# Performance work log

Hardware: AMD Instinct MI355X
Metric: run time of the kernel (lower is better)

## Reference

```python
import jax, jax.numpy as jnp
import numpy as np

D_MODEL = 1024
NUM_HEADS = 16
HEAD_DIM = D_MODEL // NUM_HEADS


def setup_inputs() -> dict:
    key = jax.random.key(0)
    k1, k2, k3, k4, k5 = jax.random.split(key, 5)
    B, S = 2, 2048
    X = jax.random.normal(k1, (B, S, D_MODEL), dtype=jnp.float32)
    Wqkv = jax.random.normal(k2, (3 * D_MODEL, D_MODEL), dtype=jnp.float32) * 0.02
    bqkv = jax.random.normal(k3, (3 * D_MODEL,), dtype=jnp.float32) * 0.02
    Wo = jax.random.normal(k4, (D_MODEL, D_MODEL), dtype=jnp.float32) * 0.02
    bo = jax.random.normal(k5, (D_MODEL,), dtype=jnp.float32) * 0.02
    return {"X": X, "Wqkv": Wqkv, "bqkv": bqkv, "Wo": Wo, "bo": bo}


def reference(X, Wqkv, bqkv, Wo, bo):
    B, S, D = X.shape
    # fused QKV projection (torch Linear: x @ W.T + b)
    qkv = X @ Wqkv.T + bqkv                                  # [B, S, 3D]
    qkv = qkv.reshape(B, S, NUM_HEADS, 3 * HEAD_DIM)
    qkv = jnp.transpose(qkv, (0, 2, 1, 3))                   # [B, H, S, 3*hd]
    q, k, v = jnp.split(qkv, 3, axis=-1)                     # each [B, H, S, hd]
    # naive scaled dot-product attention (materializes full SxS scores)
    scale = 1.0 / jnp.sqrt(jnp.asarray(HEAD_DIM, dtype=X.dtype))
    scores = jnp.einsum("bhqd,bhkd->bhqk", q, k) * scale     # [B, H, S, S]
    attn = jax.nn.softmax(scores, axis=-1)
    values = jnp.einsum("bhqk,bhkd->bhqd", attn, v)          # [B, H, S, hd]
    values = jnp.transpose(values, (0, 2, 1, 3)).reshape(B, S, D)
    return values @ Wo.T + bo
```

## Files before the change

### kernel.cpp

```cpp
#include <hip/hip_runtime.h>

#define DM    1024
#define NH    16
#define HD    64
#define SEQ   2048
#define BATCH 2
#define NQKV  3072
#define MTOT  4096

using half2v = __attribute__((ext_vector_type(2))) _Float16;
using half4  = __attribute__((ext_vector_type(4))) _Float16;
using half8  = __attribute__((ext_vector_type(8))) _Float16;
using f32x4  = __attribute__((ext_vector_type(4))) float;

typedef const __attribute__((address_space(1))) unsigned int* gp_t;
typedef __attribute__((address_space(3))) unsigned int* lp_t;

__device__ __forceinline__ void gl2lds16(const void* g, void* l) {
    __builtin_amdgcn_global_load_lds((gp_t)g, (lp_t)l, 16, 0, 0);
}

__device__ __forceinline__ f32x4 fzero4() {
    f32x4 v; v[0] = 0.f; v[1] = 0.f; v[2] = 0.f; v[3] = 0.f; return v;
}

__device__ __forceinline__ int sw8(int row, int col) {
    return (row << 6) | ((((col >> 3) ^ row) & 7) << 3) | (col & 7);
}

#define CSCALE 0.18033688011112042f

__device__ __forceinline__ half2v expp2(float a, float b) {
    return __builtin_bit_cast(half2v, __builtin_amdgcn_cvt_pkrtz(
        __builtin_amdgcn_exp2f(a), __builtin_amdgcn_exp2f(b)));
}

__global__ __launch_bounds__(256) void cvt_all(const float* __restrict__ X,
                                               const float* __restrict__ W1,
                                               const float* __restrict__ W2,
                                               const float* __restrict__ bqkv,
                                               float* __restrict__ bscaled,
                                               _Float16* __restrict__ out) {
    const int nX = MTOT * DM / 4, nW1 = NQKV * DM / 4, nW2 = DM * DM / 4;
    int i = blockIdx.x * 256 + threadIdx.x;
    if (i < NQKV) {
        const float b = bqkv[i];
        bscaled[i] = ((i % 192) < 64) ? b * CSCALE : b;
    }
    if (i >= nX + nW1 + nW2) return;
    float4 f;
    float sc = 1.0f;
    if (i < nX) {
        f = reinterpret_cast<const float4*>(X)[i];
    } else if (i < nX + nW1) {
        const int off = i - nX;
        f = reinterpret_cast<const float4*>(W1)[off];
        const int row = off >> 8;
        if ((row % 192) < 64) sc = CSCALE;
    } else {
        f = reinterpret_cast<const float4*>(W2)[i - nX - nW1];
    }
    half4 h;
    h[0] = (_Float16)(f.x * sc); h[1] = (_Float16)(f.y * sc);
    h[2] = (_Float16)(f.z * sc); h[3] = (_Float16)(f.w * sc);
    reinterpret_cast<half4*>(out)[i] = h;
}

template <bool OUT_F16, bool FUSE_V>
__global__ __launch_bounds__(256) void gemm_nt(const _Float16* __restrict__ A,
                                               const _Float16* __restrict__ B,
                                               const float* __restrict__ bias,
                                               void* __restrict__ Cout,
                                               _Float16* __restrict__ vtout,
                                               int M, int N, int K) {
    __shared__ _Float16 lA[128 * 64];
    __shared__ _Float16 lB[128 * 64];
    const int tid = threadIdx.x;
    const int m0 = blockIdx.y * 128, n0 = blockIdx.x * 128;
    const int wave = tid >> 6, lane = tid & 63, quad = lane >> 4, l15 = lane & 15;
    const int wm = (wave & 1) * 64, wn = (wave >> 1) * 64;

    f32x4 acc[4][4];
#pragma unroll
    for (int i = 0; i < 4; ++i)
#pragma unroll
        for (int j = 0; j < 4; ++j) acc[i][j] = fzero4();

    const int cperm = (((tid & 7) ^ (tid >> 3)) & 7) * 8;
    const _Float16* Ab = A + (long)(m0 + (tid >> 3)) * K + cperm;
    const _Float16* Bb = B + (long)(n0 + (tid >> 3)) * K + cperm;
    char* lAp = (char*)lA + tid * 16;
    char* lBp = (char*)lB + tid * 16;

    for (int kt = 0; kt < K; kt += 64) {
        __syncthreads();
#pragma unroll
        for (int j = 0; j < 4; ++j) {
            gl2lds16(Ab + (long)j * 32 * K + kt, lAp + j * 4096);
            gl2lds16(Bb + (long)j * 32 * K + kt, lBp + j * 4096);
        }
        __syncthreads();
#pragma unroll
        for (int ks = 0; ks < 2; ++ks) {
            half8 af[4], bfr[4];
#pragma unroll
            for (int t = 0; t < 4; ++t) {
                af[t]  = *(const half8*)(lA + sw8(wm + t * 16 + l15, ks * 32 + quad * 8));
                bfr[t] = *(const half8*)(lB + sw8(wn + t * 16 + l15, ks * 32 + quad * 8));
            }
#pragma unroll
            for (int mt = 0; mt < 4; ++mt)
#pragma unroll
                for (int nt = 0; nt < 4; ++nt)
                    acc[mt][nt] = __builtin_amdgcn_mfma_f32_16x16x32_f16(
                        af[mt], bfr[nt], acc[mt][nt], 0, 0, 0);
        }
    }

    float bs[4];
#pragma unroll
    for (int nt = 0; nt < 4; ++nt) bs[nt] = bias[n0 + wn + nt * 16 + l15];

#pragma unroll
    for (int nt = 0; nt < 4; ++nt) {
        const int nbase = n0 + wn + nt * 16;
        if (FUSE_V && (nbase % 192) >= 128) {
            const int h = nbase / 192;
            const int d = (nbase % 192) - 128 + l15;
            _Float16* vrow = vtout + ((long)((nbase / 192) * 0 + h) * HD + d) * SEQ;
#pragma unroll
            for (int mt = 0; mt < 4; ++mt) {
                const int mbase = m0 + wm + mt * 16;
                const int bb = mbase >> 11;
                const int sbase = mbase & (SEQ - 1);
                const int pos = (sbase & ~31) + 8 * quad + 4 * ((sbase >> 4) & 1);
                half4 hv;
#pragma unroll
                for (int r = 0; r < 4; ++r) hv[r] = (_Float16)(acc[mt][nt][r] + bs[nt]);
                *(half4*)(vrow + (long)bb * NH * HD * SEQ + pos) = hv;
            }
        } else {
#pragma unroll
            for (int mt = 0; mt < 4; ++mt) {
#pragma unroll
                for (int r = 0; r < 4; ++r) {
                    const int m = m0 + wm + mt * 16 + quad * 4 + r;
                    const int n = nbase + l15;
                    const float v = acc[mt][nt][r] + bs[nt];
                    if constexpr (OUT_F16)
                        ((_Float16*)Cout)[(long)m * N + n] = (_Float16)v;
                    else
                        ((float*)Cout)[(long)m * N + n] = v;
                }
            }
        }
    }
}

template <bool OUT_F16>
__global__ __launch_bounds__(256) void gemm_nt_64(const _Float16* __restrict__ A,
                                                  const _Float16* __restrict__ B,
                                                  const float* __restrict__ bias,
                                                  void* __restrict__ Cout,
                                                  int M, int N, int K) {
    __shared__ _Float16 lA[64 * 64];
    __shared__ _Float16 lB[128 * 64];
    const int tid = threadIdx.x;
    const int m0 = blockIdx.y * 64, n0 = blockIdx.x * 128;
    const int wave = tid >> 6, lane = tid & 63, quad = lane >> 4, l15 = lane & 15;
    const int wm = (wave & 1) * 32, wn = (wave >> 1) * 64;

    f32x4 acc[2][4];
#pragma unroll
    for (int i = 0; i < 2; ++i)
#pragma unroll
        for (int j = 0; j < 4; ++j) acc[i][j] = fzero4();

    const int cperm = (((tid & 7) ^ (tid >> 3)) & 7) * 8;
    const _Float16* Ab = A + (long)(m0 + (tid >> 3)) * K + cperm;
    const _Float16* Bb = B + (long)(n0 + (tid >> 3)) * K + cperm;
    char* lAp = (char*)lA + tid * 16;
    char* lBp = (char*)lB + tid * 16;

    for (int kt = 0; kt < K; kt += 64) {
        __syncthreads();
#pragma unroll
        for (int j = 0; j < 2; ++j)
            gl2lds16(Ab + (long)j * 32 * K + kt, lAp + j * 4096);
#pragma unroll
        for (int j = 0; j < 4; ++j)
            gl2lds16(Bb + (long)j * 32 * K + kt, lBp + j * 4096);
        __syncthreads();
#pragma unroll
        for (int ks = 0; ks < 2; ++ks) {
            half8 af[2], bfr[4];
#pragma unroll
            for (int t = 0; t < 2; ++t)
                af[t] = *(const half8*)(lA + sw8(wm + t * 16 + l15, ks * 32 + quad * 8));
#pragma unroll
            for (int t = 0; t < 4; ++t)
                bfr[t] = *(const half8*)(lB + sw8(wn + t * 16 + l15, ks * 32 + quad * 8));
#pragma unroll
            for (int mt = 0; mt < 2; ++mt)
#pragma unroll
                for (int nt = 0; nt < 4; ++nt)
                    acc[mt][nt] = __builtin_amdgcn_mfma_f32_16x16x32_f16(
                        af[mt], bfr[nt], acc[mt][nt], 0, 0, 0);
        }
    }

    float bs[4];
#pragma unroll
    for (int nt = 0; nt < 4; ++nt) bs[nt] = bias[n0 + wn + nt * 16 + l15];

#pragma unroll
    for (int mt = 0; mt < 2; ++mt) {
#pragma unroll
        for (int r = 0; r < 4; ++r) {
            const int m = m0 + wm + mt * 16 + quad * 4 + r;
#pragma unroll
            for (int nt = 0; nt < 4; ++nt) {
                const int n = n0 + wn + nt * 16 + l15;
                const float v = acc[mt][nt][r] + bs[nt];
                if constexpr (OUT_F16)
                    ((_Float16*)Cout)[(long)m * N + n] = (_Float16)v;
                else
                    ((float*)Cout)[(long)m * N + n] = v;
            }
        }
    }
}

__global__ __launch_bounds__(256) void attn_flash(const _Float16* __restrict__ qkv,
                                                  const _Float16* __restrict__ vt,
                                                  _Float16* __restrict__ aout) {
    __shared__ _Float16 lKV[4][64 * 64];

    const int L = blockIdx.x;
    const int c = L & 7, j = L >> 3;
    const int pair = c * 4 + (j >> 5);
    const int b = pair >> 4, h = pair & 15;
    const int q0 = (j & 31) * 64;

    const int tid = threadIdx.x;
    const int wave = tid >> 6, lane = tid & 63, quad = lane >> 4, l15 = lane & 15;
    const int cperm8 = (((tid & 7) ^ (tid >> 3)) & 7) * 8;

    const _Float16* qsrc = qkv + (long)(b * SEQ + q0 + (tid >> 3)) * NQKV + h * 192 + cperm8;
#pragma unroll
    for (int jq = 0; jq < 2; ++jq)
        gl2lds16(qsrc + (long)jq * 32 * NQKV, (char*)lKV + jq * 4096 + tid * 16);
    __syncthreads();

    half8 qf[2];
#pragma unroll
    for (int ks = 0; ks < 2; ++ks)
        qf[ks] = *(const half8*)(lKV[0] + sw8(wave * 16 + l15, ks * 32 + quad * 8));
    __syncthreads();

    f32x4 O[4];
#pragma unroll
    for (int dt = 0; dt < 4; ++dt) O[dt] = fzero4();
    f32x4 lsum = fzero4();

    half8 ones;
#pragma unroll
    for (int i = 0; i < 8; ++i) ones[i] = (_Float16)1.0f;

    const _Float16* ksrc = qkv + (long)(b * SEQ + (tid >> 3)) * NQKV + h * 192 + 64 + cperm8;
    const _Float16* vsrc = vt + (long)((b * NH + h) * HD + (tid >> 3)) * SEQ + cperm8;

#pragma unroll
    for (int jj = 0; jj < 2; ++jj) {
        gl2lds16(ksrc + (long)(jj * 32) * NQKV, (char*)lKV[0] + jj * 4096 + tid * 16);
        gl2lds16(vsrc + (long)(jj * 32) * SEQ,  (char*)lKV[2] + jj * 4096 + tid * 16);
    }
    __syncthreads();

    for (int it = 0; it < 32; ++it) {
        const int cur = it & 1;
        if (it < 31) {
            const int s0n = (it + 1) * 64;
#pragma unroll
            for (int jj = 0; jj < 2; ++jj) {
                gl2lds16(ksrc + (long)(s0n + jj * 32) * NQKV, (char*)lKV[cur ^ 1] + jj * 4096 + tid * 16);
                gl2lds16(vsrc + (long)(jj * 32) * SEQ + s0n,  (char*)lKV[2 + (cur ^ 1)] + jj * 4096 + tid * 16);
            }
        }
        const _Float16* lK = lKV[cur];
        const _Float16* lV = lKV[2 + cur];

#pragma unroll
        for (int t = 0; t < 2; ++t) {
            f32x4 s[2];
            s[0] = fzero4(); s[1] = fzero4();
#pragma unroll
            for (int tt = 0; tt < 2; ++tt) {
#pragma unroll
                for (int ks = 0; ks < 2; ++ks) {
                    half8 kf = *(const half8*)(lK + sw8((2 * t + tt) * 16 + l15, ks * 32 + quad * 8));
                    s[tt] = __builtin_amdgcn_mfma_f32_16x16x32_f16(kf, qf[ks], s[tt], 0, 0, 0);
                }
            }
            half2v p01 = expp2(s[0][0], s[0][1]);
            half2v p23 = expp2(s[0][2], s[0][3]);
            half2v p45 = expp2(s[1][0], s[1][1]);
            half2v p67 = expp2(s[1][2], s[1][3]);
            half4 lo = __builtin_shufflevector(p01, p23, 0, 1, 2, 3);
            half4 hi = __builtin_shufflevector(p45, p67, 0, 1, 2, 3);
            half8 pf = __builtin_shufflevector(lo, hi, 0, 1, 2, 3, 4, 5, 6, 7);
            lsum = __builtin_amdgcn_mfma_f32_16x16x32_f16(pf, ones, lsum, 0, 0, 0);
#pragma unroll
            for (int dt = 0; dt < 4; ++dt) {
                half8 vf = *(const half8*)(lV + sw8(dt * 16 + l15, t * 32 + quad * 8));
                O[dt] = __builtin_amdgcn_mfma_f32_16x16x32_f16(pf, vf, O[dt], 0, 0, 0);
            }
        }
        __syncthreads();
    }

#pragma unroll
    for (int r = 0; r < 4; ++r) {
        const float lr = 1.0f / lsum[r];
        const int row = b * SEQ + q0 + wave * 16 + quad * 4 + r;
#pragma unroll
        for (int dt = 0; dt < 4; ++dt)
            aout[(long)row * DM + h * HD + dt * 16 + l15] =
                (_Float16)(O[dt][r] * lr);
    }
}

extern "C" void kernel_launch(void* const* d_in, const int* in_sizes, int n_in,
                              void* d_out, int out_size, void* d_ws, size_t ws_size,
                              hipStream_t stream) {
    const float* X    = (const float*)d_in[0];
    const float* Wqkv = (const float*)d_in[1];
    const float* bqkv = (const float*)d_in[2];
    const float* Wo   = (const float*)d_in[3];
    const float* bo   = (const float*)d_in[4];

    char* ws = (char*)d_ws;
    _Float16* Xh   = (_Float16*)(ws);
    _Float16* Wqh  = (_Float16*)(ws + (size_t)8  * 1048576);
    _Float16* Woh  = (_Float16*)(ws + (size_t)14 * 1048576);
    _Float16* qkvh = (_Float16*)(ws + (size_t)16 * 1048576);
    _Float16* vth  = (_Float16*)(ws + (size_t)40 * 1048576);
    _Float16* atth = (_Float16*)(ws + (size_t)48 * 1048576);
    float* bscaled = (float*)(ws + (size_t)48 * 1048576);

    const int ncvt = (MTOT * DM + NQKV * DM + DM * DM) / 4;
    cvt_all<<<(ncvt + 255) / 256, 256, 0, stream>>>(X, Wqkv, Wo, bqkv, bscaled, Xh);

    gemm_nt<true, true><<<dim3(NQKV / 128, MTOT / 128), 256, 0, stream>>>(
        Xh, Wqh, bscaled, qkvh, vth, MTOT, NQKV, DM);

    attn_flash<<<1024, 256, 0, stream>>>(qkvh, vth, atth);

    gemm_nt_64<false><<<dim3(DM / 128, MTOT / 64), 256, 0, stream>>>(
        atth, Woh, bo, d_out, MTOT, DM, DM);
}
```

Baseline: 187.2 us.

## Switch attention kernel to 32x32x16 MFMA with split-K across wave pairs

Rewrites the flash attention inner loop to use 32x32x16 MFMA tiles. Each pair of waves shares a 32-row query tile and splits each 64-key block in half, and the two partial O and row-sum accumulators are reduced through LDS at the end. The V-transpose layout written by the QKV GEMM epilogue is changed to match the new B-operand fragment order. The aim is to cut LDS fragment reads and instruction count per FLOP, at the cost of a final cross-wave reduction, more accumulator registers, and only half the waves doing the output stores.

```diff
diff --git a/kernel.cpp b/kernel.cpp
--- a/kernel.cpp
+++ b/kernel.cpp
@@ -12,6 +12,7 @@
 using half4  = __attribute__((ext_vector_type(4))) _Float16;
 using half8  = __attribute__((ext_vector_type(8))) _Float16;
 using f32x4  = __attribute__((ext_vector_type(4))) float;
+using f32x16 = __attribute__((ext_vector_type(16))) float;
 
 typedef const __attribute__((address_space(1))) unsigned int* gp_t;
 typedef __attribute__((address_space(3))) unsigned int* lp_t;
@@ -22,6 +23,12 @@
 
 __device__ __forceinline__ f32x4 fzero4() {
     f32x4 v; v[0] = 0.f; v[1] = 0.f; v[2] = 0.f; v[3] = 0.f; return v;
+}
+__device__ __forceinline__ f32x16 fzero16() {
+    f32x16 v;
+#pragma unroll
+    for (int i = 0; i < 16; ++i) v[i] = 0.f;
+    return v;
 }
 
 __device__ __forceinline__ int sw8(int row, int col) {
@@ -127,13 +134,13 @@
         if (FUSE_V && (nbase % 192) >= 128) {
             const int h = nbase / 192;
             const int d = (nbase % 192) - 128 + l15;
-            _Float16* vrow = vtout + ((long)((nbase / 192) * 0 + h) * HD + d) * SEQ;
+            _Float16* vrow = vtout + ((long)h * HD + d) * SEQ;
 #pragma unroll
             for (int mt = 0; mt < 4; ++mt) {
                 const int mbase = m0 + wm + mt * 16;
                 const int bb = mbase >> 11;
                 const int sbase = mbase & (SEQ - 1);
-                const int pos = (sbase & ~31) + 8 * quad + 4 * ((sbase >> 4) & 1);
+                const int pos = sbase + 8 * (quad & 1) + 4 * (quad >> 1);
                 half4 hv;
 #pragma unroll
                 for (int r = 0; r < 4; ++r) hv[r] = (_Float16)(acc[mt][nt][r] + bs[nt]);
@@ -243,7 +250,9 @@
     const int q0 = (j & 31) * 64;
 
     const int tid = threadIdx.x;
-    const int wave = tid >> 6, lane = tid & 63, quad = lane >> 4, l15 = lane & 15;
+    const int wave = tid >> 6, lane = tid & 63;
+    const int l31 = lane & 31, hi = lane >> 5;
+    const int qt = wave >> 1, kh = wave & 1;
     const int cperm8 = (((tid & 7) ^ (tid >> 3)) & 7) * 8;
 
     const _Float16* qsrc = qkv + (long)(b * SEQ + q0 + (tid >> 3)) * NQKV + h * 192 + cperm8;
@@ -252,16 +261,14 @@
         gl2lds16(qsrc + (long)jq * 32 * NQKV, (char*)lKV + jq * 4096 + tid * 16);
     __syncthreads();
 
-    half8 qf[2];
-#pragma unroll
-    for (int ks = 0; ks < 2; ++ks)
-        qf[ks] = *(const half8*)(lKV[0] + sw8(wave * 16 + l15, ks * 32 + quad * 8));
+    half8 qf[4];
+#pragma unroll
+    for (int ks = 0; ks < 4; ++ks)
+        qf[ks] = *(const half8*)(lKV[0] + sw8(32 * qt + l31, ks * 16 + hi * 8));
     __syncthreads();
 
-    f32x4 O[4];
-#pragma unroll
-    for (int dt = 0; dt < 4; ++dt) O[dt] = fzero4();
-    f32x4 lsum = fzero4();
+    f32x16 O[2] = {fzero16(), fzero16()};
+    f32x16 lsum = fzero16();
 
     half8 ones;
 #pragma unroll
@@ -290,43 +297,76 @@
         const _Float16* lK = lKV[cur];
         const _Float16* lV = lKV[2 + cur];
 
-#pragma unroll
-        for (int t = 0; t < 2; ++t) {
-            f32x4 s[2];
-            s[0] = fzero4(); s[1] = fzero4();
-#pragma unroll
-            for (int tt = 0; tt < 2; ++tt) {
-#pragma unroll
-                for (int ks = 0; ks < 2; ++ks) {
-                    half8 kf = *(const half8*)(lK + sw8((2 * t + tt) * 16 + l15, ks * 32 + quad * 8));
-                    s[tt] = __builtin_amdgcn_mfma_f32_16x16x32_f16(kf, qf[ks], s[tt], 0, 0, 0);
-                }
-            }
-            half2v p01 = expp2(s[0][0], s[0][1]);
-            half2v p23 = expp2(s[0][2], s[0][3]);
-            half2v p45 = expp2(s[1][0], s[1][1]);
-            half2v p67 = expp2(s[1][2], s[1][3]);
+        f32x16 st = fzero16();
+#pragma unroll
+        for (int ks = 0; ks < 4; ++ks) {
+            half8 kf = *(const half8*)(lK + sw8(32 * kh + l31, ks * 16 + hi * 8));
+            st = __builtin_amdgcn_mfma_f32_32x32x16_f16(kf, qf[ks], st, 0, 0, 0);
+        }
+
+#pragma unroll
+        for (int kc = 0; kc < 2; ++kc) {
+            half2v p01 = expp2(st[8 * kc + 0], st[8 * kc + 1]);
+            half2v p23 = expp2(st[8 * kc + 2], st[8 * kc + 3]);
+            half2v p45 = expp2(st[8 * kc + 4], st[8 * kc + 5]);
+            half2v p67 = expp2(st[8 * kc + 6], st[8 * kc + 7]);
             half4 lo = __builtin_shufflevector(p01, p23, 0, 1, 2, 3);
-            half4 hi = __builtin_shufflevector(p45, p67, 0, 1, 2, 3);
-            half8 pf = __builtin_shufflevector(lo, hi, 0, 1, 2, 3, 4, 5, 6, 7);
-            lsum = __builtin_amdgcn_mfma_f32_16x16x32_f16(pf, ones, lsum, 0, 0, 0);
-#pragma unroll
-            for (int dt = 0; dt < 4; ++dt) {
-                half8 vf = *(const half8*)(lV + sw8(dt * 16 + l15, t * 32 + quad * 8));
-                O[dt] = __builtin_amdgcn_mfma_f32_16x16x32_f16(pf, vf, O[dt], 0, 0, 0);
+            half4 hp = __builtin_shufflevector(p45, p67, 0, 1, 2, 3);
+            half8 pf = __builtin_shufflevector(lo, hp, 0, 1, 2, 3, 4, 5, 6, 7);
+            lsum = __builtin_amdgcn_mfma_f32_32x32x16_f16(pf, ones, lsum, 0, 0, 0);
+#pragma unroll
+            for (int dt = 0; dt < 2; ++dt) {
+                half8 vf = *(const half8*)(lV + sw8(32 * dt + l31, kh * 32 + kc * 16 + hi * 8));
+                O[dt] = __builtin_amdgcn_mfma_f32_32x32x16_f16(pf, vf, O[dt], 0, 0, 0);
             }
         }
         __syncthreads();
     }
 
-#pragma unroll
-    for (int r = 0; r < 4; ++r) {
-        const float lr = 1.0f / lsum[r];
-        const int row = b * SEQ + q0 + wave * 16 + quad * 4 + r;
-#pragma unroll
-        for (int dt = 0; dt < 4; ++dt)
-            aout[(long)row * DM + h * HD + dt * 16 + l15] =
-                (_Float16)(O[dt][r] * lr);
+    float* red = (float*)lKV;
+    if (kh) {
+#pragma unroll
+        for (int dt = 0; dt < 2; ++dt)
+#pragma unroll
+            for (int cc = 0; cc < 4; ++cc) {
+                f32x4 v;
+#pragma unroll
+                for (int i = 0; i < 4; ++i) v[i] = O[dt][4 * cc + i];
+                *(f32x4*)(red + ((qt * 12 + dt * 4 + cc) * 256) + lane * 4) = v;
+            }
+#pragma unroll
+        for (int cc = 0; cc < 4; ++cc) {
+            f32x4 v;
+#pragma unroll
+            for (int i = 0; i < 4; ++i) v[i] = lsum[4 * cc + i];
+            *(f32x4*)(red + ((qt * 12 + 8 + cc) * 256) + lane * 4) = v;
+        }
+    }
+    __syncthreads();
+    if (!kh) {
+#pragma unroll
+        for (int dt = 0; dt < 2; ++dt)
+#pragma unroll
+            for (int cc = 0; cc < 4; ++cc) {
+                f32x4 v = *(const f32x4*)(red + ((qt * 12 + dt * 4 + cc) * 256) + lane * 4);
+#pragma unroll
+                for (int i = 0; i < 4; ++i) O[dt][4 * cc + i] += v[i];
+            }
+#pragma unroll
+        for (int cc = 0; cc < 4; ++cc) {
+            f32x4 v = *(const f32x4*)(red + ((qt * 12 + 8 + cc) * 256) + lane * 4);
+#pragma unroll
+            for (int i = 0; i < 4; ++i) lsum[4 * cc + i] += v[i];
+        }
+#pragma unroll
+        for (int r = 0; r < 16; ++r) {
+            const float lr = 1.0f / lsum[r];
+            const int row = b * SEQ + q0 + 32 * qt + (r & 3) + 8 * (r >> 2) + 4 * hi;
+#pragma unroll
+            for (int dt = 0; dt < 2; ++dt)
+                aout[(long)row * DM + h * HD + 32 * dt + l31] =
+                    (_Float16)(O[dt][r] * lr);
+        }
     }
 }
 
```

Result: slower. 193.7 us (+3.4%).

## Double-buffer LDS tiles in GEMMs and shrink QKV GEMM M-tile to 64

Applied to the files above, without the earlier changes.

Replaces both GEMM kernels with one double-buffered variant that prefetches the next K-slice into a second LDS buffer while MFMAs run on the current one, leaving one barrier per iteration. The QKV projection moves from 128x128 to 64x128 tiles, which doubles its block count and lowers per-block accumulator registers. In exchange, each block reuses its loaded B tile across fewer rows, so global and L2 traffic rises, and LDS per block grows to hold two buffers.

```diff
diff --git a/kernel.cpp b/kernel.cpp
--- a/kernel.cpp
+++ b/kernel.cpp
@@ -67,54 +67,66 @@
 }
 
 template <bool OUT_F16, bool FUSE_V>
-__global__ __launch_bounds__(256) void gemm_nt(const _Float16* __restrict__ A,
+__global__ __launch_bounds__(256) void gemm_db(const _Float16* __restrict__ A,
                                                const _Float16* __restrict__ B,
                                                const float* __restrict__ bias,
                                                void* __restrict__ Cout,
                                                _Float16* __restrict__ vtout,
                                                int M, int N, int K) {
-    __shared__ _Float16 lA[128 * 64];
-    __shared__ _Float16 lB[128 * 64];
+    __shared__ _Float16 lA[2][64 * 64];
+    __shared__ _Float16 lB[2][128 * 64];
     const int tid = threadIdx.x;
-    const int m0 = blockIdx.y * 128, n0 = blockIdx.x * 128;
+    const int m0 = blockIdx.y * 64, n0 = blockIdx.x * 128;
     const int wave = tid >> 6, lane = tid & 63, quad = lane >> 4, l15 = lane & 15;
-    const int wm = (wave & 1) * 64, wn = (wave >> 1) * 64;
-
-    f32x4 acc[4][4];
-#pragma unroll
-    for (int i = 0; i < 4; ++i)
+    const int wm = (wave & 1) * 32, wn = (wave >> 1) * 64;
+
+    f32x4 acc[2][4];
+#pragma unroll
+    for (int i = 0; i < 2; ++i)
 #pragma unroll
         for (int j = 0; j < 4; ++j) acc[i][j] = fzero4();
 
     const int cperm = (((tid & 7) ^ (tid >> 3)) & 7) * 8;
     const _Float16* Ab = A + (long)(m0 + (tid >> 3)) * K + cperm;
     const _Float16* Bb = B + (long)(n0 + (tid >> 3)) * K + cperm;
-    char* lAp = (char*)lA + tid * 16;
-    char* lBp = (char*)lB + tid * 16;
-
-    for (int kt = 0; kt < K; kt += 64) {
-        __syncthreads();
-#pragma unroll
-        for (int j = 0; j < 4; ++j) {
-            gl2lds16(Ab + (long)j * 32 * K + kt, lAp + j * 4096);
-            gl2lds16(Bb + (long)j * 32 * K + kt, lBp + j * 4096);
-        }
-        __syncthreads();
+
+#pragma unroll
+    for (int j = 0; j < 2; ++j)
+        gl2lds16(Ab + (long)j * 32 * K, (char*)lA[0] + j * 4096 + tid * 16);
+#pragma unroll
+    for (int j = 0; j < 4; ++j)
+        gl2lds16(Bb + (long)j * 32 * K, (char*)lB[0] + j * 4096 + tid * 16);
+    __syncthreads();
+
+    const int KI = K >> 6;
+    for (int it = 0; it < KI; ++it) {
+        const int cur = it & 1;
+        if (it + 1 < KI) {
+            const int kt = (it + 1) * 64;
+#pragma unroll
+            for (int j = 0; j < 2; ++j)
+                gl2lds16(Ab + (long)j * 32 * K + kt, (char*)lA[cur ^ 1] + j * 4096 + tid * 16);
+#pragma unroll
+            for (int j = 0; j < 4; ++j)
+                gl2lds16(Bb + (long)j * 32 * K + kt, (char*)lB[cur ^ 1] + j * 4096 + tid * 16);
+        }
 #pragma unroll
         for (int ks = 0; ks < 2; ++ks) {
-            half8 af[4], bfr[4];
-#pragma unroll
-            for (int t = 0; t < 4; ++t) {
-                af[t]  = *(const half8*)(lA + sw8(wm + t * 16 + l15, ks * 32 + quad * 8));
-                bfr[t] = *(const half8*)(lB + sw8(wn + t * 16 + l15, ks * 32 + quad * 8));
-            }
-#pragma unroll
-            for (int mt = 0; mt < 4; ++mt)
+            half8 af[2], bfr[4];
+#pragma unroll
+            for (int t = 0; t < 2; ++t)
+                af[t] = *(const half8*)(lA[cur] + sw8(wm + t * 16 + l15, ks * 32 + quad * 8));
+#pragma unroll
+            for (int t = 0; t < 4; ++t)
+                bfr[t] = *(const half8*)(lB[cur] + sw8(wn + t * 16 + l15, ks * 32 + quad * 8));
+#pragma unroll
+            for (int mt = 0; mt < 2; ++mt)
 #pragma unroll
                 for (int nt = 0; nt < 4; ++nt)
                     acc[mt][nt] = __builtin_amdgcn_mfma_f32_16x16x32_f16(
                         af[mt], bfr[nt], acc[mt][nt], 0, 0, 0);
         }
+        __syncthreads();
     }
 
     float bs[4];
@@ -127,9 +139,9 @@
         if (FUSE_V && (nbase % 192) >= 128) {
             const int h = nbase / 192;
             const int d = (nbase % 192) - 128 + l15;
-            _Float16* vrow = vtout + ((long)((nbase / 192) * 0 + h) * HD + d) * SEQ;
-#pragma unroll
-            for (int mt = 0; mt < 4; ++mt) {
+            _Float16* vrow = vtout + ((long)h * HD + d) * SEQ;
+#pragma unroll
+            for (int mt = 0; mt < 2; ++mt) {
                 const int mbase = m0 + wm + mt * 16;
                 const int bb = mbase >> 11;
                 const int sbase = mbase & (SEQ - 1);
@@ -141,7 +153,7 @@
             }
         } else {
 #pragma unroll
-            for (int mt = 0; mt < 4; ++mt) {
+            for (int mt = 0; mt < 2; ++mt) {
 #pragma unroll
                 for (int r = 0; r < 4; ++r) {
                     const int m = m0 + wm + mt * 16 + quad * 4 + r;
@@ -157,80 +169,6 @@
     }
 }
 
-template <bool OUT_F16>
-__global__ __launch_bounds__(256) void gemm_nt_64(const _Float16* __restrict__ A,
-                                                  const _Float16* __restrict__ B,
-                                                  const float* __restrict__ bias,
-                                                  void* __restrict__ Cout,
-                                                  int M, int N, int K) {
-    __shared__ _Float16 lA[64 * 64];
-    __shared__ _Float16 lB[128 * 64];
-    const int tid = threadIdx.x;
-    const int m0 = blockIdx.y * 64, n0 = blockIdx.x * 128;
-    const int wave = tid >> 6, lane = tid & 63, quad = lane >> 4, l15 = lane & 15;
-    const int wm = (wave & 1) * 32, wn = (wave >> 1) * 64;
-
-    f32x4 acc[2][4];
-#pragma unroll
-    for (int i = 0; i < 2; ++i)
-#pragma unroll
-        for (int j = 0; j < 4; ++j) acc[i][j] = fzero4();
-
-    const int cperm = (((tid & 7) ^ (tid >> 3)) & 7) * 8;
-    const _Float16* Ab = A + (long)(m0 + (tid >> 3)) * K + cperm;
-    const _Float16* Bb = B + (long)(n0 + (tid >> 3)) * K + cperm;
-    char* lAp = (char*)lA + tid * 16;
-    char* lBp = (char*)lB + tid * 16;
-
-    for (int kt = 0; kt < K; kt += 64) {
-        __syncthreads();
-#pragma unroll
-        for (int j = 0; j < 2; ++j)
-            gl2lds16(Ab + (long)j * 32 * K + kt, lAp + j * 4096);
-#pragma unroll
-        for (int j = 0; j < 4; ++j)
-            gl2lds16(Bb + (long)j * 32 * K + kt, lBp + j * 4096);
-        __syncthreads();
-#pragma unroll
-        for (int ks = 0; ks < 2; ++ks) {
-            half8 af[2], bfr[4];
-#pragma unroll
-            for (int t = 0; t < 2; ++t)
-                af[t] = *(const half8*)(lA + sw8(wm + t * 16 + l15, ks * 32 + quad * 8));
-#pragma unroll
-            for (int t = 0; t < 4; ++t)
-                bfr[t] = *(const half8*)(lB + sw8(wn + t * 16 + l15, ks * 32 + quad * 8));
-#pragma unroll
-            for (int mt = 0; mt < 2; ++mt)
-#pragma unroll
-                for (int nt = 0; nt < 4; ++nt)
-                    acc[mt][nt] = __builtin_amdgcn_mfma_f32_16x16x32_f16(
-                        af[mt], bfr[nt], acc[mt][nt], 0, 0, 0);
-        }
-    }
-
-    float bs[4];
-#pragma unroll
-    for (int nt = 0; nt < 4; ++nt) bs[nt] = bias[n0 + wn + nt * 16 + l15];
-
-#pragma unroll
-    for (int mt = 0; mt < 2; ++mt) {
-#pragma unroll
-        for (int r = 0; r < 4; ++r) {
-            const int m = m0 + wm + mt * 16 + quad * 4 + r;
-#pragma unroll
-            for (int nt = 0; nt < 4; ++nt) {
-                const int n = n0 + wn + nt * 16 + l15;
-                const float v = acc[mt][nt][r] + bs[nt];
-                if constexpr (OUT_F16)
-                    ((_Float16*)Cout)[(long)m * N + n] = (_Float16)v;
-                else
-                    ((float*)Cout)[(long)m * N + n] = v;
-            }
-        }
-    }
-}
-
 __global__ __launch_bounds__(256) void attn_flash(const _Float16* __restrict__ qkv,
                                                   const _Float16* __restrict__ vt,
                                                   _Float16* __restrict__ aout) {
@@ -351,11 +289,11 @@
     const int ncvt = (MTOT * DM + NQKV * DM + DM * DM) / 4;
     cvt_all<<<(ncvt + 255) / 256, 256, 0, stream>>>(X, Wqkv, Wo, bqkv, bscaled, Xh);
 
-    gemm_nt<true, true><<<dim3(NQKV / 128, MTOT / 128), 256, 0, stream>>>(
+    gemm_db<true, true><<<dim3(NQKV / 128, MTOT / 64), 256, 0, stream>>>(
         Xh, Wqh, bscaled, qkvh, vth, MTOT, NQKV, DM);
 
     attn_flash<<<1024, 256, 0, stream>>>(qkvh, vth, atth);
 
-    gemm_nt_64<false><<<dim3(DM / 128, MTOT / 64), 256, 0, stream>>>(
-        atth, Woh, bo, d_out, MTOT, DM, DM);
-}
+    gemm_db<false, false><<<dim3(DM / 128, MTOT / 64), 256, 0, stream>>>(
+        atth, Woh, bo, d_out, nullptr, MTOT, DM, DM);
+}
```

After: 190.5 us. No clear change (+1.8%).
